# Kernel tuning notes

Hardware: AMD Instinct MI355X
Metric: run time of the kernel (lower is better)

The kernel has to match this reference:

```python
import jax, jax.numpy as jnp
import numpy as np

B, S, H = 4, 1024, 4096
NH, NKV, HD = 32, 8, 128
LEVEL = 256


def lsq_quant(x, s, sym):
    # LSQ fake quantization with grad-scale on s and STE round.
    if sym:
        qn, qp = -LEVEL // 2, LEVEL // 2 - 1
    else:
        qn, qp = 0, LEVEL - 1
    g = 1.0 / np.sqrt(x.size * qp)
    s_sc = s * g + jax.lax.stop_gradient(s - s * g)  # value == s, grad scaled by g
    xs = jnp.clip(x / s_sc, qn, qp)
    xq = xs + jax.lax.stop_gradient(jnp.round(xs) - xs)  # STE round
    return xq * s_sc


def rotate_half(x):
    d = x.shape[-1] // 2
    return jnp.concatenate([-x[..., d:], x[..., :d]], axis=-1)


def setup_inputs() -> dict:
    key = jax.random.key(0)
    ks = jax.random.split(key, 8)
    hidden_states = jax.random.normal(ks[0], (B, S, H), dtype=jnp.float32)
    # real RoPE tables (theta=10000)
    inv_freq = 1.0 / (10000.0 ** (np.arange(0, HD, 2, dtype=np.float32) / HD))
    pos = np.arange(S, dtype=np.float32)
    freqs = np.outer(pos, inv_freq)                      # [S, HD/2]
    emb = np.concatenate([freqs, freqs], axis=-1)        # [S, HD]
    cos = jnp.broadcast_to(jnp.cos(emb)[None], (B, S, HD)).astype(jnp.float32)
    sin = jnp.broadcast_to(jnp.sin(emb)[None], (B, S, HD)).astype(jnp.float32)
    # additive causal mask [B,1,S,S]
    neg = jnp.finfo(jnp.float32).min
    causal = jnp.where(jnp.tril(jnp.ones((S, S), bool)), 0.0, neg)
    attention_mask = jnp.broadcast_to(causal[None, None], (B, 1, S, S)).astype(jnp.float32)
    std = 1.0 / np.sqrt(H)
    Wq = jax.random.normal(ks[1], (NH * HD, H), dtype=jnp.float32) * std
    Wk = jax.random.normal(ks[2], (NKV * HD, H), dtype=jnp.float32) * std
    Wv = jax.random.normal(ks[3], (NKV * HD, H), dtype=jnp.float32) * std
    Wo = jax.random.normal(ks[4], (H, NH * HD), dtype=jnp.float32) * std
    return {
        "hidden_states": hidden_states, "cos": cos, "sin": sin,
        "attention_mask": attention_mask,
        "Wq": Wq, "Wk": Wk, "Wv": Wv, "Wo": Wo,
        "s_q": jnp.float32(0.05), "s_k": jnp.float32(0.05), "s_v": jnp.float32(0.05),
        "s_attn": jnp.float32(0.05), "s_after": jnp.float32(0.05), "s_o": jnp.float32(0.05),
    }


def reference(hidden_states, cos, sin, attention_mask, Wq, Wk, Wv, Wo,
              s_q, s_k, s_v, s_attn, s_after, s_o):
    b, s, _ = hidden_states.shape
    scaling = HD ** -0.5
    n_rep = NH // NKV
    # projections (torch Linear: x @ W^T), reshape to [B, heads, S, HD]
    q = (hidden_states @ Wq.T).reshape(b, s, NH, HD).transpose(0, 2, 1, 3)
    k = (hidden_states @ Wk.T).reshape(b, s, NKV, HD).transpose(0, 2, 1, 3)
    v = (hidden_states @ Wv.T).reshape(b, s, NKV, HD).transpose(0, 2, 1, 3)
    q = lsq_quant(q, s_q, sym=True)
    k = lsq_quant(k, s_k, sym=True)
    v = lsq_quant(v, s_v, sym=True)
    # rotary embeddings (cos/sin: [B,S,HD] -> broadcast over head dim)
    c = cos[:, None, :, :]
    sn = sin[:, None, :, :]
    q = q * c + rotate_half(q) * sn
    k = k * c + rotate_half(k) * sn
    # repeat KV heads for GQA
    k = jnp.repeat(k, n_rep, axis=1)
    v = jnp.repeat(v, n_rep, axis=1)
    attn = jnp.einsum('bhqd,bhkd->bhqk', q, k) * scaling
    attn = lsq_quant(attn, s_attn, sym=False)
    attn = attn + attention_mask
    attn = jax.nn.softmax(attn.astype(jnp.float32), axis=-1)
    out = jnp.einsum('bhqk,bhkd->bhqd', attn, v)
    out = lsq_quant(out, s_after, sym=False)
    out = out.transpose(0, 2, 1, 3).reshape(b, s, NH * HD)
    out = out @ Wo.T
    out = lsq_quant(out, s_o, sym=True)
    return out, attn
```

## Files before the change

kernel.cpp:

```cpp
#include <hip/hip_runtime.h>
#include <math.h>

#define B_   4
#define S_   1024
#define H_   4096
#define NH_  32
#define NKV_ 8
#define HD_  128
#define M_   (B_*S_)
#define SCALING 0.08838834764831845f

#define R16M 16777216

typedef _Float16 f16;
typedef __attribute__((ext_vector_type(4))) _Float16 f16x4;
typedef __attribute__((ext_vector_type(8))) _Float16 f16x8;
typedef __attribute__((ext_vector_type(4))) float f32x4;

__device__ __forceinline__ float lsq_sym(float x, float s) {
  float xs = x / s;
  xs = fminf(fmaxf(xs, -128.0f), 127.0f);
  return rintf(xs) * s;
}
__device__ __forceinline__ float lsq_asym(float x, float s) {
  float xs = x / s;
  xs = fminf(fmaxf(xs, 0.0f), 255.0f);
  return rintf(xs) * s;
}

struct f16pair { f16 hi, lo; };
__device__ __forceinline__ f16pair cvt_hilo(float x) {
  f16pair r;
  r.hi = (f16)x;
  r.lo = (f16)(x - (float)r.hi);
  return r;
}

__device__ __forceinline__ void gload16(const void* g, void* l) {
  __builtin_amdgcn_global_load_lds((const __attribute__((address_space(1))) void*)g,
                                   (__attribute__((address_space(3))) void*)l, 16, 0, 0);
}

__global__ __launch_bounds__(256)
void split_flat(const float* __restrict__ src, f16* __restrict__ hi, f16* __restrict__ lo)
{
  const size_t i = ((size_t)blockIdx.x * 256 + threadIdx.x) * 4;
  float4 v = *(const float4*)(src + i);
  f16x4 h, l; f16pair p;
  p = cvt_hilo(v.x); h.x = p.hi; l.x = p.lo;
  p = cvt_hilo(v.y); h.y = p.hi; l.y = p.lo;
  p = cvt_hilo(v.z); h.z = p.hi; l.z = p.lo;
  p = cvt_hilo(v.w); h.w = p.hi; l.w = p.lo;
  *(f16x4*)(hi + i) = h;
  *(f16x4*)(lo + i) = l;
}

__global__ __launch_bounds__(256)
void split_wqk(const float* __restrict__ W, f16* __restrict__ hi, f16* __restrict__ lo)
{
  const size_t i = ((size_t)blockIdx.x * 256 + threadIdx.x) * 4;
  const int n = (int)(i >> 12);
  const int k = (int)(i & 4095);
  const int d = n & 127;
  const int prow = (n & ~127) | ((d < 64) ? (d << 1) : (((d - 64) << 1) | 1));
  float4 v = *(const float4*)(W + i);
  f16x4 h, l; f16pair p;
  p = cvt_hilo(v.x); h.x = p.hi; l.x = p.lo;
  p = cvt_hilo(v.y); h.y = p.hi; l.y = p.lo;
  p = cvt_hilo(v.z); h.z = p.hi; l.z = p.lo;
  p = cvt_hilo(v.w); h.w = p.hi; l.w = p.lo;
  *(f16x4*)(hi + (size_t)prow * 4096 + k) = h;
  *(f16x4*)(lo + (size_t)prow * 4096 + k) = l;
}

template<int BM, int ATERMS, int EPI>
__global__ __launch_bounds__(256, 2)
void gemm_mfma(const f16* __restrict__ Ahi, const f16* __restrict__ Alo, int lda,
               const f16* __restrict__ Bhi, const f16* __restrict__ Blo, int ldb,
               float* __restrict__ C, int ldc, int K,
               const float* __restrict__ sQp, const float* __restrict__ sKp,
               const float* __restrict__ sVp,
               const float* __restrict__ cosp, const float* __restrict__ sinp,
               f16* __restrict__ qhi, f16* __restrict__ qlo,
               f16* __restrict__ kfrag, f16* __restrict__ vt)
{
  constexpr int MI  = BM >> 5;
  constexpr int AIT = BM >> 6;

  __shared__ f16 sAh[BM * 32];
  __shared__ f16 sAl[(ATERMS == 2) ? BM * 32 : 64];
  __shared__ f16 sBh[128 * 32];
  __shared__ f16 sBl[128 * 32];

  const int m0 = blockIdx.y * BM;
  const int n0 = blockIdx.x << 7;
  const int t    = threadIdx.x;
  const int lane = t & 63;
  const int wv   = t >> 6;
  const int wm   = (wv >> 1) * (BM >> 1);
  const int wn   = (wv & 1) << 6;
  const int lrow = lane & 15;
  const int kg   = (lane >> 4) << 3;
  const int fsw  = (lrow & 3) << 3;

  const int sr   = lane >> 2;
  const int slot = lane & 3;
  const int kcs  = ((slot ^ (sr & 3)) << 3);

  f32x4 acc[MI][4];
  #pragma unroll
  for (int i = 0; i < MI; ++i)
    #pragma unroll
    for (int j = 0; j < 4; ++j) acc[i][j] = (f32x4){0.f, 0.f, 0.f, 0.f};

  for (int k0 = 0; k0 < K; k0 += 32) {
    #pragma unroll
    for (int i = 0; i < AIT; ++i) {
      const int rowb = wv * (BM >> 2) + (i << 4);
      const size_t goff = (size_t)(m0 + rowb + sr) * lda + k0 + kcs;
      gload16(Ahi + goff, &sAh[rowb * 32]);
      if constexpr (ATERMS == 2) gload16(Alo + goff, &sAl[rowb * 32]);
    }
    #pragma unroll
    for (int i = 0; i < 2; ++i) {
      const int rowb = (wv << 5) + (i << 4);
      const size_t goff = (size_t)(n0 + rowb + sr) * ldb + k0 + kcs;
      gload16(Bhi + goff, &sBh[rowb * 32]);
      gload16(Blo + goff, &sBl[rowb * 32]);
    }
    __syncthreads();

    f16x8 a[MI], bh[4], bl[4];
    #pragma unroll
    for (int j = 0; j < 4; ++j) {
      const int r = wn + (j << 4) + lrow;
      bh[j] = *(const f16x8*)&sBh[r * 32 + (kg ^ fsw)];
      bl[j] = *(const f16x8*)&sBl[r * 32 + (kg ^ fsw)];
    }
    #pragma unroll
    for (int i = 0; i < MI; ++i)
      a[i] = *(const f16x8*)&sAh[(wm + (i << 4) + lrow) * 32 + (kg ^ fsw)];
    #pragma unroll
    for (int i = 0; i < MI; ++i)
      #pragma unroll
      for (int j = 0; j < 4; ++j) {
        acc[i][j] = __builtin_amdgcn_mfma_f32_16x16x32_f16(a[i], bh[j], acc[i][j], 0, 0, 0);
        acc[i][j] = __builtin_amdgcn_mfma_f32_16x16x32_f16(a[i], bl[j], acc[i][j], 0, 0, 0);
      }
    if constexpr (ATERMS == 2) {
      #pragma unroll
      for (int i = 0; i < MI; ++i)
        a[i] = *(const f16x8*)&sAl[(wm + (i << 4) + lrow) * 32 + (kg ^ fsw)];
      #pragma unroll
      for (int i = 0; i < MI; ++i)
        #pragma unroll
        for (int j = 0; j < 4; ++j)
          acc[i][j] = __builtin_amdgcn_mfma_f32_16x16x32_f16(a[i], bh[j], acc[i][j], 0, 0, 0);
    }
    __syncthreads();
  }

  int region = 0;
  float s, sQv = 1.0f;
  if constexpr (EPI == 1) {
    s = *sQp; sQv = *sKp;
  } else {
    region = (n0 < 4096) ? 0 : ((n0 < 5120) ? 1 : 2);
    s = (region == 0) ? *sQp : (region == 1) ? *sKp : *sVp;
  }

  #pragma unroll
  for (int i = 0; i < MI; ++i)
    #pragma unroll
    for (int j = 0; j < 4; ++j) {
      const int gc = n0 + wn + (j << 4) + lrow;
      #pragma unroll
      for (int r = 0; r < 4; ++r) {
        const int gr = m0 + wm + (i << 4) + ((lane >> 4) << 2) + r;
        float x = acc[i][j][r];
        if constexpr (EPI == 1) {
          C[(size_t)gr * ldc + gc] = lsq_sym(x * s, sQv);
        } else {
          if (region <= 1) {
            float qv = lsq_sym(x, s);
            float pv = __shfl_xor(qv, 1);
            const int dperm = gc & 127;
            const int dpair = dperm >> 1;
            float cs = cosp[(size_t)gr * HD_ + dpair];
            float sn = sinp[(size_t)gr * HD_ + dpair];
            float ro = (gc & 1) ? (qv * cs + pv * sn) : (qv * cs - pv * sn);
            f16pair hp = cvt_hilo(ro);
            if (region == 0) {
              qhi[(size_t)gr * 4096 + gc] = hp.hi;
              qlo[(size_t)gr * 4096 + gc] = hp.lo;
            } else {
              const int lcol = gc - 4096;
              const int bb = gr >> 10, ki = gr & 1023;
              const int kvh = lcol >> 7;
              const int c = dperm >> 5, sub = (dperm >> 3) & 3, e = dperm & 7;
              const size_t base = ((size_t)(bb * 8 + kvh) << 18) + ((size_t)(ki >> 4) << 12)
                                + (c << 10) + ((ki & 15) << 3) + (sub << 7) + e;
              kfrag[base] = hp.hi;
              kfrag[base + 512] = hp.lo;
            }
          } else {
            float xi = rintf(fminf(fmaxf(x / s, -128.0f), 127.0f));
            const int lcol = gc - 5120;
            const int bb = gr >> 10, ss = gr & 1023;
            const int kv = lcol >> 7, dd = lcol & 127;
            vt[(((size_t)(bb * 8 + kv) * 128 + dd) << 10) + ss] = (f16)xi;
          }
        }
      }
    }
}

__global__ __launch_bounds__(256)
void attn_fused(const f16* __restrict__ qhiB, const f16* __restrict__ qloB,
                const f16* __restrict__ kfrag, float* __restrict__ attn,
                const float* __restrict__ saP)
{
  const int b = blockIdx.z, h = blockIdx.y, qi0 = blockIdx.x << 4;
  const int t = threadIdx.x, lane = t & 63, w = t >> 6;
  const int lc = lane & 15, lg = lane >> 4;
  const int kvh = h >> 2;
  const float sa = *saP;

  f16x8 qh[4], ql[4];
  {
    const size_t qoff = (size_t)(b * S_ + qi0 + lc) * 4096 + h * HD_;
    #pragma unroll
    for (int c = 0; c < 4; ++c) {
      const int off = c * 32 + lg * 8;
      qh[c] = *(const f16x8*)(qhiB + qoff + off);
      ql[c] = *(const f16x8*)(qloB + qoff + off);
    }
  }

  f32x4 acc[16];
  #pragma unroll
  for (int tt = 0; tt < 16; ++tt) acc[tt] = (f32x4){0.f, 0.f, 0.f, 0.f};

  const int qimax = qi0 + 15;
  const f16* kb = kfrag + ((size_t)(b * 8 + kvh) << 18);

  #pragma unroll
  for (int tt = 0; tt < 16; ++tt) {
    const int ki0 = (w << 8) + (tt << 4);
    if (ki0 <= qimax) {
      const f16* kt = kb + ((size_t)((w << 4) + tt) << 12) + lane * 8;
      #pragma unroll
      for (int c = 0; c < 4; ++c) {
        f16x8 kh = *(const f16x8*)(kt + (c << 10));
        f16x8 kl = *(const f16x8*)(kt + (c << 10) + 512);
        acc[tt] = __builtin_amdgcn_mfma_f32_16x16x32_f16(kh, qh[c], acc[tt], 0, 0, 0);
        acc[tt] = __builtin_amdgcn_mfma_f32_16x16x32_f16(kh, ql[c], acc[tt], 0, 0, 0);
        acc[tt] = __builtin_amdgcn_mfma_f32_16x16x32_f16(kl, qh[c], acc[tt], 0, 0, 0);
      }
    }
  }

  const int qi = qi0 + lc;

  float m = -3.0e38f;
  #pragma unroll
  for (int tt = 0; tt < 16; ++tt) {
    const int kib = (w << 8) + (tt << 4) + (lg << 2);
    #pragma unroll
    for (int r = 0; r < 4; ++r) {
      float x = (kib + r <= qi) ? lsq_asym(acc[tt][r] * SCALING, sa) : -3.0e38f;
      acc[tt][r] = x;
      m = fmaxf(m, x);
    }
  }
  m = fmaxf(m, __shfl_xor(m, 16));
  m = fmaxf(m, __shfl_xor(m, 32));

  __shared__ float redM[4][16];
  __shared__ float redS[4][16];
  if (lg == 0) redM[w][lc] = m;
  __syncthreads();
  float mrow = fmaxf(fmaxf(redM[0][lc], redM[1][lc]), fmaxf(redM[2][lc], redM[3][lc]));

  float ssum = 0.f;
  #pragma unroll
  for (int tt = 0; tt < 16; ++tt) {
    #pragma unroll
    for (int r = 0; r < 4; ++r) {
      float p = __expf(acc[tt][r] - mrow);
      acc[tt][r] = p;
      ssum += p;
    }
  }
  ssum += __shfl_xor(ssum, 16);
  ssum += __shfl_xor(ssum, 32);
  if (lg == 0) redS[w][lc] = ssum;
  __syncthreads();
  const float inv = 1.0f / (redS[0][lc] + redS[1][lc] + redS[2][lc] + redS[3][lc]);

  float* orow = attn + ((size_t)(b * NH_ + h) * S_ + qi) * S_ + (w << 8) + (lg << 2);
  #pragma unroll
  for (int tt = 0; tt < 16; ++tt) {
    float4 v;
    v.x = acc[tt][0] * inv;
    v.y = acc[tt][1] * inv;
    v.z = acc[tt][2] * inv;
    v.w = acc[tt][3] * inv;
    *(float4*)(orow + (tt << 4)) = v;
  }
}

__global__ __launch_bounds__(256)
void pv_mfma(const float* __restrict__ attn, const f16* __restrict__ vt,
             f16* __restrict__ pvint,
             const float* __restrict__ svP, const float* __restrict__ safP)
{
  const int b = blockIdx.z, h = blockIdx.y, q0 = blockIdx.x << 7;
  const int t = threadIdx.x, lane = t & 63, w = t >> 6;
  const int wd = (w >> 1) << 6, wq = (w & 1) << 6;
  const int lc = lane & 15, lg = lane >> 4;
  const int kvh = h >> 2;
  const float sv = *svP, saf = *safP;

  f32x4 acc[4][4];
  #pragma unroll
  for (int i = 0; i < 4; ++i)
    #pragma unroll
    for (int j = 0; j < 4; ++j) acc[i][j] = (f32x4){0.f, 0.f, 0.f, 0.f};

  const float* Pbase = attn + (size_t)(b * NH_ + h) * S_ * S_;
  const int kimax = q0 + 128;

  for (int ki0 = 0; ki0 < kimax; ki0 += 32) {
    f16x8 a[4];
    #pragma unroll
    for (int i = 0; i < 4; ++i) {
      const int d = wd + i * 16 + lc;
      a[i] = *(const f16x8*)(vt + (((size_t)(b * 8 + kvh) * 128 + d) << 10) + ki0 + lg * 8);
    }
    #pragma unroll
    for (int j = 0; j < 4; ++j) {
      const int q = q0 + wq + j * 16 + lc;
      const float* pp = Pbase + (size_t)q * S_ + ki0 + lg * 8;
      float4 p0 = *(const float4*)pp;
      float4 p1 = *(const float4*)(pp + 4);
      f16x8 bh, bl; f16pair pr;
      pr = cvt_hilo(p0.x); bh[0] = pr.hi; bl[0] = pr.lo;
      pr = cvt_hilo(p0.y); bh[1] = pr.hi; bl[1] = pr.lo;
      pr = cvt_hilo(p0.z); bh[2] = pr.hi; bl[2] = pr.lo;
      pr = cvt_hilo(p0.w); bh[3] = pr.hi; bl[3] = pr.lo;
      pr = cvt_hilo(p1.x); bh[4] = pr.hi; bl[4] = pr.lo;
      pr = cvt_hilo(p1.y); bh[5] = pr.hi; bl[5] = pr.lo;
      pr = cvt_hilo(p1.z); bh[6] = pr.hi; bl[6] = pr.lo;
      pr = cvt_hilo(p1.w); bh[7] = pr.hi; bl[7] = pr.lo;
      #pragma unroll
      for (int i = 0; i < 4; ++i) {
        acc[i][j] = __builtin_amdgcn_mfma_f32_16x16x32_f16(a[i], bh, acc[i][j], 0, 0, 0);
        acc[i][j] = __builtin_amdgcn_mfma_f32_16x16x32_f16(a[i], bl, acc[i][j], 0, 0, 0);
      }
    }
  }

  #pragma unroll
  for (int i = 0; i < 4; ++i)
    #pragma unroll
    for (int j = 0; j < 4; ++j) {
      const int q  = q0 + wq + j * 16 + lc;
      const int d0 = wd + i * 16 + lg * 4;
      f16x4 v;
      #pragma unroll
      for (int r = 0; r < 4; ++r) {
        float x = sv * acc[i][j][r];
        x = fminf(fmaxf(x / saf, 0.0f), 255.0f);
        v[r] = (f16)rintf(x);
      }
      *(f16x4*)(pvint + (size_t)(b * S_ + q) * 4096 + h * HD_ + d0) = v;
    }
}

extern "C" void kernel_launch(void* const* d_in, const int* in_sizes, int n_in,
                              void* d_out, int out_size, void* d_ws, size_t ws_size,
                              hipStream_t stream)
{
  const float* hidden = (const float*)d_in[0];
  const float* cosp   = (const float*)d_in[1];
  const float* sinp   = (const float*)d_in[2];
  const float* Wq     = (const float*)d_in[4];
  const float* Wk     = (const float*)d_in[5];
  const float* Wv     = (const float*)d_in[6];
  const float* Wo     = (const float*)d_in[7];
  const float* s_q    = (const float*)d_in[8];
  const float* s_k    = (const float*)d_in[9];
  const float* s_v    = (const float*)d_in[10];
  const float* s_attn = (const float*)d_in[11];
  const float* s_after= (const float*)d_in[12];
  const float* s_o    = (const float*)d_in[13];

  float* out  = (float*)d_out;
  float* attn = out + (size_t)M_ * H_;

  f16* wsf   = (f16*)d_ws;
  f16* Qhi   = wsf;
  f16* Qlo   = wsf + (size_t)R16M;
  f16* Kfrag = wsf + (size_t)2*R16M;
  f16* Vt    = wsf + (size_t)2*R16M + (size_t)R16M/2;
  f16* PVint = wsf;
  f16* WoHi  = wsf + (size_t)R16M;
  f16* WoLo  = wsf + (size_t)2*R16M;

  f16* scr = (f16*)attn;
  f16* hHi   = scr;
  f16* hLo   = scr + (size_t)R16M;
  f16* WcatH = scr + (size_t)2*R16M;
  f16* WcatL = scr + (size_t)2*R16M + (size_t)6144*4096;

  dim3 blk(256, 1, 1);

  split_flat<<<dim3(16384), blk, 0, stream>>>(hidden, hHi, hLo);
  split_wqk <<<dim3(16384), blk, 0, stream>>>(Wq, WcatH, WcatL);
  split_wqk <<<dim3(4096),  blk, 0, stream>>>(Wk, WcatH + (size_t)4096*4096, WcatL + (size_t)4096*4096);
  split_flat<<<dim3(4096),  blk, 0, stream>>>(Wv, WcatH + (size_t)5120*4096, WcatL + (size_t)5120*4096);

  gemm_mfma<128,2,5><<<dim3(48,32), blk, 0, stream>>>(hHi, hLo, H_, WcatH, WcatL, H_,
      nullptr, 0, H_, s_q, s_k, s_v, cosp, sinp, Qhi, Qlo, Kfrag, Vt);

  attn_fused<<<dim3(64, NH_, B_), blk, 0, stream>>>(Qhi, Qlo, Kfrag, attn, s_attn);

  pv_mfma<<<dim3(8, NH_, B_), blk, 0, stream>>>(attn, Vt, PVint, s_v, s_after);

  split_flat<<<dim3(16384), blk, 0, stream>>>(Wo, WoHi, WoLo);
  gemm_mfma<256,1,1><<<dim3(32,16), blk, 0, stream>>>(PVint, nullptr, 4096,
      WoHi, WoLo, 4096, out, H_, H_, s_after, s_o, nullptr, nullptr, nullptr,
      nullptr, nullptr, nullptr, nullptr);
}
```

Before: 1.513 ms.

## Double-buffer GEMM LDS tiles to overlap global loads with MFMA compute

The GEMM main loop now uses two LDS buffers per operand. It issues the direct-to-LDS loads for the next K tile before computing on the current one, with explicit vmcnt waits and raw s_barrier replacing __syncthreads. The aim is to hide global-memory latency behind the MFMA work instead of stalling at each tile. This doubles LDS use per block, which may cut occupancy. The fixed vmcnt(8) assumes each stage issues exactly 8 loads; template instantiations that issue fewer per stage could read a tile before it has arrived.

```diff
diff --git a/kernel.cpp b/kernel.cpp
--- a/kernel.cpp
+++ b/kernel.cpp
@@ -86,11 +86,13 @@
 {
   constexpr int MI  = BM >> 5;
   constexpr int AIT = BM >> 6;
-
-  __shared__ f16 sAh[BM * 32];
-  __shared__ f16 sAl[(ATERMS == 2) ? BM * 32 : 64];
-  __shared__ f16 sBh[128 * 32];
-  __shared__ f16 sBl[128 * 32];
+  constexpr int ASZ = BM * 32;
+  constexpr int BSZ = 128 * 32;
+
+  __shared__ f16 sAh[2 * ASZ];
+  __shared__ f16 sAl[(ATERMS == 2) ? 2 * ASZ : 64];
+  __shared__ f16 sBh[2 * BSZ];
+  __shared__ f16 sBl[2 * BSZ];
 
   const int m0 = blockIdx.y * BM;
   const int n0 = blockIdx.x << 7;
@@ -107,39 +109,56 @@
   const int slot = lane & 3;
   const int kcs  = ((slot ^ (sr & 3)) << 3);
 
-  f32x4 acc[MI][4];
-  #pragma unroll
-  for (int i = 0; i < MI; ++i)
-    #pragma unroll
-    for (int j = 0; j < 4; ++j) acc[i][j] = (f32x4){0.f, 0.f, 0.f, 0.f};
-
-  for (int k0 = 0; k0 < K; k0 += 32) {
+  auto STAGE = [&](int kt, int buf) {
+    const int k0 = kt << 5;
+    const int ao = buf * ASZ, bo = buf * BSZ;
     #pragma unroll
     for (int i = 0; i < AIT; ++i) {
       const int rowb = wv * (BM >> 2) + (i << 4);
       const size_t goff = (size_t)(m0 + rowb + sr) * lda + k0 + kcs;
-      gload16(Ahi + goff, &sAh[rowb * 32]);
-      if constexpr (ATERMS == 2) gload16(Alo + goff, &sAl[rowb * 32]);
+      gload16(Ahi + goff, &sAh[ao + rowb * 32]);
+      if constexpr (ATERMS == 2) gload16(Alo + goff, &sAl[ao + rowb * 32]);
     }
     #pragma unroll
     for (int i = 0; i < 2; ++i) {
       const int rowb = (wv << 5) + (i << 4);
       const size_t goff = (size_t)(n0 + rowb + sr) * ldb + k0 + kcs;
-      gload16(Bhi + goff, &sBh[rowb * 32]);
-      gload16(Blo + goff, &sBl[rowb * 32]);
-    }
-    __syncthreads();
-
+      gload16(Bhi + goff, &sBh[bo + rowb * 32]);
+      gload16(Blo + goff, &sBl[bo + rowb * 32]);
+    }
+  };
+
+  f32x4 acc[MI][4];
+  #pragma unroll
+  for (int i = 0; i < MI; ++i)
+    #pragma unroll
+    for (int j = 0; j < 4; ++j) acc[i][j] = (f32x4){0.f, 0.f, 0.f, 0.f};
+
+  const int T = K >> 5;
+  STAGE(0, 0);
+
+  for (int kt = 0; kt < T; ++kt) {
+    const int cur = kt & 1;
+    if (kt + 1 < T) {
+      STAGE(kt + 1, cur ^ 1);
+      asm volatile("s_waitcnt vmcnt(8)" ::: "memory");
+    } else {
+      asm volatile("s_waitcnt vmcnt(0)" ::: "memory");
+    }
+    __builtin_amdgcn_sched_barrier(0);
+    asm volatile("s_barrier" ::: "memory");
+
+    const int ao = cur * ASZ, bo = cur * BSZ;
     f16x8 a[MI], bh[4], bl[4];
     #pragma unroll
     for (int j = 0; j < 4; ++j) {
       const int r = wn + (j << 4) + lrow;
-      bh[j] = *(const f16x8*)&sBh[r * 32 + (kg ^ fsw)];
-      bl[j] = *(const f16x8*)&sBl[r * 32 + (kg ^ fsw)];
+      bh[j] = *(const f16x8*)&sBh[bo + r * 32 + (kg ^ fsw)];
+      bl[j] = *(const f16x8*)&sBl[bo + r * 32 + (kg ^ fsw)];
     }
     #pragma unroll
     for (int i = 0; i < MI; ++i)
-      a[i] = *(const f16x8*)&sAh[(wm + (i << 4) + lrow) * 32 + (kg ^ fsw)];
+      a[i] = *(const f16x8*)&sAh[ao + (wm + (i << 4) + lrow) * 32 + (kg ^ fsw)];
     #pragma unroll
     for (int i = 0; i < MI; ++i)
       #pragma unroll
@@ -150,14 +169,17 @@
     if constexpr (ATERMS == 2) {
       #pragma unroll
       for (int i = 0; i < MI; ++i)
-        a[i] = *(const f16x8*)&sAl[(wm + (i << 4) + lrow) * 32 + (kg ^ fsw)];
+        a[i] = *(const f16x8*)&sAl[ao + (wm + (i << 4) + lrow) * 32 + (kg ^ fsw)];
       #pragma unroll
       for (int i = 0; i < MI; ++i)
         #pragma unroll
         for (int j = 0; j < 4; ++j)
           acc[i][j] = __builtin_amdgcn_mfma_f32_16x16x32_f16(a[i], bh[j], acc[i][j], 0, 0, 0);
     }
-    __syncthreads();
+
+    asm volatile("s_waitcnt lgkmcnt(0)" ::: "memory");
+    __builtin_amdgcn_sched_barrier(0);
+    asm volatile("s_barrier" ::: "memory");
   }
 
   int region = 0;
```

After: 1.511 ms. About the same (-0.1%).
